# Kernel optimization log

Hardware: AMD Instinct MI355X
Metric: run time of the kernel (lower is better)

Reference implementation:

```python
import jax, jax.numpy as jnp
import numpy as np
import math

B, S, D, H = 16, 256, 1024, 16
DK = D // H
MAXLEN = 512


def _sinusoid_table(maxlen, dim):
    # rows for positions -maxlen .. maxlen-1  (2*maxlen rows)
    pos = jnp.arange(-maxlen, maxlen, dtype=jnp.float32)[:, None]
    i = jnp.arange(dim)
    angle = pos / jnp.power(10000.0, (2 * (i // 2)) / dim).astype(jnp.float32)
    return jnp.where(i % 2 == 0, jnp.sin(angle), jnp.cos(angle))


def setup_inputs() -> dict:
    key = jax.random.key(0)
    ks = jax.random.split(key, 13)
    std_qk = math.sqrt(2.0 / (D + DK))
    inp = {
        "x": jax.random.normal(ks[0], (B, S, D), jnp.float32),
        "Wq": jax.random.normal(ks[1], (D, D), jnp.float32) * std_qk,
        "bq": jnp.zeros((D,), jnp.float32),
        "Wk": jax.random.normal(ks[2], (D, D), jnp.float32) * std_qk,
        "bk": jnp.zeros((D,), jnp.float32),
        "Wv": jax.random.normal(ks[3], (D, D), jnp.float32) * std_qk,
        "bv": jnp.zeros((D,), jnp.float32),
        "Wr": jax.random.normal(ks[4], (D, D), jnp.float32) * std_qk,
        "br": jnp.zeros((D,), jnp.float32),
        "u_bias": jax.random.normal(ks[5], (H, DK), jnp.float32) * math.sqrt(2.0 / (H + DK)),
        "v_bias": jax.random.normal(ks[6], (H, DK), jnp.float32) * math.sqrt(2.0 / (H + DK)),
        "Wo": jax.random.normal(ks[7], (D, D), jnp.float32) * math.sqrt(2.0 / (D + D)),
        "bo": jnp.zeros((D,), jnp.float32),
    }
    return inp


def reference(x, Wq, bq, Wk, bk, Wv, bv, Wr, br, u_bias, v_bias, Wo, bo):
    table = _sinusoid_table(MAXLEN, D)  # (2*MAXLEN, D)
    # relative position indices: idx[s, z] = z - s, shifted by +MAXLEN
    relpos_idx = (jnp.arange(2 * S)[None, :] - jnp.arange(S)[:, None])[:, :S] + MAXLEN
    relpos_vec = table[relpos_idx]  # (S, S, D)

    q = (x @ Wq.T + bq).reshape(B, S, H, DK)
    k = (x @ Wk.T + bk).reshape(B, S, H, DK)
    v = (x @ Wv.T + bv).reshape(B, S, H, DK)

    rp_k = (relpos_vec @ Wk.T + bk).reshape(S, S, H, DK)       # shared k_proj
    kR = (x @ Wr.T + br).reshape(B, S, H, DK)                  # relpos_k_proj(keys)
    rp_R = (relpos_vec @ Wr.T + br).reshape(S, S, H, DK)       # relpos_k_proj(relpos)

    w = jnp.einsum('bshd,bzhd->bhsz', q, k)
    w = w + jnp.einsum('bshd,szhd->bhsz', q, rp_k)
    w = w + jnp.einsum('hd,bzhd->bhz', u_bias, kR)[:, :, None, :]
    w = w + jnp.einsum('hd,szhd->hsz', v_bias, rp_R)[None, :, :, :]
    w = w / math.sqrt(DK)

    causal = jnp.tril(jnp.ones((S, S), jnp.float32))[None, None, :, :]
    w = w + jnp.log(causal)  # -inf above diagonal

    attn = jax.nn.softmax(w, axis=-1)                          # (B,H,S,S)
    vw = jnp.einsum('bhsz,bzhd->bshd', attn, v).reshape(B, S, D)
    return vw @ Wo.T + bo
```

## Files before the change

kernel.cpp:

```cpp
#include <hip/hip_runtime.h>
#include <math.h>

constexpr int kB  = 16;
constexpr int kS  = 256;
constexpr int kD  = 1024;
constexpr int kH  = 16;
constexpr float kScale = 0.125f;

using bf16x8  = __attribute__((ext_vector_type(8))) short;
using floatx4 = __attribute__((ext_vector_type(4))) float;
typedef unsigned short u16;

__device__ __forceinline__ u16 f2bf(float x) {
  union { float f; unsigned u; } v; v.f = x;
  unsigned r = v.u + 0x7fffu + ((v.u >> 16) & 1u);
  return (u16)(r >> 16);
}
__device__ __forceinline__ float bf2f(u16 h) {
  union { unsigned u; float f; } v; v.u = ((unsigned)h) << 16;
  return v.f;
}

#define MFMA16(a, b, c) __builtin_amdgcn_mfma_f32_16x16x32_bf16((a), (b), (c), 0, 0, 0)
#define GLL16(gp, lp)                                                        \
  __builtin_amdgcn_global_load_lds(                                          \
      (const __attribute__((address_space(1))) unsigned int*)(gp),           \
      (__attribute__((address_space(3))) unsigned int*)(lp), 16, 0, 0)

__global__ __launch_bounds__(256) void pack_k(
    const float* __restrict__ x, const float* __restrict__ Wq,
    const float* __restrict__ Wk, const float* __restrict__ Wv,
    const float* __restrict__ Wo,
    const float* __restrict__ bq, const float* __restrict__ bk,
    const float* __restrict__ bv,
    const float* __restrict__ Wr, const float* __restrict__ br,
    const float* __restrict__ ub, const float* __restrict__ vb,
    u16* __restrict__ xA, u16* __restrict__ W3b, u16* __restrict__ Wob,
    float* __restrict__ b3) {
  if (blockIdx.x >= 8451) {
    int gid = (blockIdx.x - 8451) * 256 + threadIdx.x;
    int j = gid >> 10, c = gid & 1023;
    int h = j & 15;
    const float* bvec = (j < 16 ? ub : vb) + h * 64;
    const float* wcol = Wr + (size_t)(h * 64) * 1024 + c;
    float a = 0.f;
#pragma unroll
    for (int d = 0; d < 64; ++d) a += bvec[d] * wcol[(size_t)d * 1024];
    W3b[(size_t)(3072 + j) * 1024 + c] = f2bf(a);
    if (gid < 128) {
      float s = 0.f;
      if (gid < 32) {
        const float* bv2 = (gid < 16 ? ub : vb) + (gid & 15) * 64;
        const float* brp = br + (gid & 15) * 64;
        for (int d = 0; d < 64; ++d) s += bv2[d] * brp[d];
      }
      b3[3072 + gid] = s;
    }
    return;
  }
  size_t i = ((size_t)blockIdx.x * 256 + threadIdx.x) * 4;
  const size_t NX = (size_t)4194304, NW = (size_t)1048576;
  const size_t BEND = NX + 4 * NW + 3072;
  const float* src;
  u16* dst;
  size_t o;
  if (i < NX) {
    src = x; dst = xA; o = i;
  } else if (i < NX + 3 * NW) {
    size_t j = i - NX;
    int sel = (int)(j >> 20);
    o = j & (NW - 1);
    src = sel == 0 ? Wq : sel == 1 ? Wv : Wk;
    dst = W3b + (size_t)sel * NW;
  } else if (i < NX + 4 * NW) {
    o = i - NX - 3 * NW;
    src = Wo; dst = Wob;
  } else if (i < BEND) {
    size_t j = i - NX - 4 * NW;
    int sel = (int)(j >> 10);
    o = j & 1023;
    src = sel == 0 ? bq : sel == 1 ? bv : bk;
    *reinterpret_cast<float4*>(b3 + j) = *reinterpret_cast<const float4*>(src + o);
    return;
  } else if (i < BEND + 262144) {
    size_t j = i - BEND;
    int p = (int)(j >> 10);
    int ibase = (int)(j & 1023);
    ushort4 r;
    u16* rr = (u16*)&r;
#pragma unroll
    for (int c = 0; c < 4; ++c) {
      int idx = ibase + c;
      float ex = (float)(2 * (idx / 2)) * (1.0f / 1024.0f);
      float scale = exp2f(ex * -13.287712379549449f);
      float angle = (float)(p - 255) * scale;
      rr[c] = f2bf((idx & 1) ? cosf(angle) : sinf(angle));
    }
    *reinterpret_cast<ushort4*>(xA + NX + j) = r;
    return;
  } else {
    return;
  }
  float4 v = *reinterpret_cast<const float4*>(src + o);
  ushort4 r;
  r.x = f2bf(v.x); r.y = f2bf(v.y); r.z = f2bf(v.z); r.w = f2bf(v.w);
  *reinterpret_cast<ushort4*>(dst + o) = r;
}

__global__ __launch_bounds__(256) void gemm_k(
    const u16* __restrict__ A, const u16* __restrict__ W,
    const float* __restrict__ bias, float* __restrict__ Cv,
    int M, int N, int K, int mTiles, int nTiles) {
  const int xcd = blockIdx.x & 7;
  const int li  = blockIdx.x >> 3;
  const int r0   = (xcd * mTiles) >> 3;
  const int rcnt = (((xcd + 1) * mTiles) >> 3) - r0;
  if (li >= rcnt * nTiles) return;
  const int bm = (r0 + li % rcnt) * 128;
  const int bn = (li / rcnt) * 128;

  __shared__ u16 Alds[2][128 * 64];
  __shared__ u16 Blds[2][128 * 64];
  const int t = threadIdx.x, w = t >> 6, l = t & 63;
  const int l15 = l & 15, quad = l >> 4;
  const int wm = w >> 1, wn = w & 1;
  const int lrow8 = l >> 3;
  const int kslot = l & 7;
  const int NT = K >> 6;

  floatx4 acc[4][4] = {};

  auto stage = [&](int kt) {
    const int buf = kt & 1, k0 = kt << 6;
#pragma unroll
    for (int sg = 0; sg < 4; ++sg) {
      int mrow = sg * 32 + w * 8 + lrow8;
      int gk = (kslot ^ (mrow & 7)) << 3;
      GLL16(A + (size_t)(bm + mrow) * K + k0 + gk, Alds[buf] + (sg * 32 + w * 8) * 64);
      GLL16(W + (size_t)(bn + mrow) * K + k0 + gk, Blds[buf] + (sg * 32 + w * 8) * 64);
    }
  };

  stage(0);
  asm volatile("s_waitcnt vmcnt(0)" ::: "memory");
  __syncthreads();

  for (int kt = 0; kt < NT; ++kt) {
    if (kt + 1 < NT) stage(kt + 1);
    const u16* AL = Alds[kt & 1];
    const u16* BL = Blds[kt & 1];
#pragma unroll
    for (int c = 0; c < 2; ++c) {
      bf16x8 af[4], bf[4];
#pragma unroll
      for (int mi = 0; mi < 4; ++mi) {
        int am = wm * 64 + mi * 16 + l15;
        af[mi] = *(const bf16x8*)(AL + am * 64 + (((c * 4 + quad) ^ (am & 7)) << 3));
      }
#pragma unroll
      for (int ni = 0; ni < 4; ++ni) {
        int an = wn * 64 + ni * 16 + l15;
        bf[ni] = *(const bf16x8*)(BL + an * 64 + (((c * 4 + quad) ^ (an & 7)) << 3));
      }
#pragma unroll
      for (int mi = 0; mi < 4; ++mi)
#pragma unroll
        for (int ni = 0; ni < 4; ++ni)
          acc[mi][ni] = MFMA16(af[mi], bf[ni], acc[mi][ni]);
    }
    asm volatile("s_waitcnt vmcnt(0)" ::: "memory");
    __syncthreads();
  }

#pragma unroll
  for (int ni = 0; ni < 4; ++ni) {
    int col = bn + wn * 64 + ni * 16 + l15;
    float bv = bias[col];
#pragma unroll
    for (int mi = 0; mi < 4; ++mi) {
      int mrow = bm + wm * 64 + mi * 16 + quad * 4;
#pragma unroll
      for (int r = 0; r < 4; ++r) {
        Cv[(size_t)(mrow + r) * N + col] = acc[mi][ni][r] + bv;
      }
    }
  }
}

#define PHASE_MFMA(aa, bb, mh, nh, LG)                                         \
  do {                                                                         \
    __builtin_amdgcn_s_barrier();                                              \
    asm volatile("s_waitcnt lgkmcnt(" #LG ")" ::: "memory");                   \
    __builtin_amdgcn_sched_barrier(0);                                         \
    __builtin_amdgcn_s_setprio(1);                                             \
    _Pragma("unroll") for (int kc = 0; kc < 2; ++kc)                           \
        _Pragma("unroll") for (int i = 0; i < 4; ++i)                          \
            _Pragma("unroll") for (int j = 0; j < 2; ++j)                      \
                acc[(mh) * 4 + i][(nh) * 2 + j] = MFMA16(                      \
                    aa[kc][i], bb[kc][j], acc[(mh) * 4 + i][(nh) * 2 + j]);    \
    __builtin_amdgcn_s_setprio(0);                                             \
  } while (0)

__global__ __launch_bounds__(512, 2) void gemm256_k(
    const u16* __restrict__ A, const u16* __restrict__ W,
    const float* __restrict__ bias, u16* __restrict__ Cv,
    int K, float* __restrict__ utb, float* __restrict__ dtb,
    int mTiles, int nTiles) {
  const int nwg = mTiles * nTiles;
  const int qq = nwg >> 3, rr8 = nwg & 7;
  const int xcd = blockIdx.x & 7;
  const int wgid = (xcd < rr8 ? xcd * (qq + 1) : rr8 * (qq + 1) + (xcd - rr8) * qq)
                   + (blockIdx.x >> 3);
  const int bm = (wgid / nTiles) * 256;
  const int bn = (wgid % nTiles) * 256;

  __shared__ u16 lds[2 * 32768];

  const int t = threadIdx.x, w = t >> 6, l = t & 63;
  const int l15 = l & 15, quad = l >> 4;
  const int wm = w >> 2, wn = w & 3;

  const int NT = K >> 6;
  floatx4 acc[8][4] = {};

  auto stage = [&](int kt, int h) {
    const u16* srcm = (h < 2) ? A : W;
    const int baser = ((h < 2) ? bm : bn) + (h & 1) * 128;
    u16* dst = lds + (kt & 1) * 32768 + h * 8192 + w * 512;
    const int k0 = kt << 6;
#pragma unroll
    for (int j = 0; j < 2; ++j) {
      int sub = w * 8 + (l >> 3) + j * 64;
      int gk = ((l & 7) ^ (sub & 7)) << 3;
      GLL16(srcm + (size_t)(baser + sub) * K + k0 + gk, dst + j * 4096);
    }
  };

  bf16x8 a0[2][4], a1[2][4], b0[2][2], b1[2][2];

  auto readA = [&](bf16x8 (&aa)[2][4], const u16* LA, int hh) {
#pragma unroll
    for (int i = 0; i < 4; ++i) {
      int am = wm * 128 + hh * 64 + i * 16 + l15;
      const u16* p = LA + am * 64;
      aa[0][i] = *(const bf16x8*)(p + ((quad ^ (am & 7)) << 3));
      aa[1][i] = *(const bf16x8*)(p + (((4 + quad) ^ (am & 7)) << 3));
    }
  };
  auto readB = [&](bf16x8 (&bb)[2][2], const u16* LB, int hh) {
#pragma unroll
    for (int j = 0; j < 2; ++j) {
      int an = wn * 64 + hh * 32 + j * 16 + l15;
      const u16* p = LB + an * 64;
      bb[0][j] = *(const bf16x8*)(p + ((quad ^ (an & 7)) << 3));
      bb[1][j] = *(const bf16x8*)(p + (((4 + quad) ^ (an & 7)) << 3));
    }
  };

  stage(0, 2); stage(0, 3); stage(0, 0); stage(0, 1);
  stage(1, 2); stage(1, 3); stage(1, 0);
  asm volatile("s_waitcnt vmcnt(6)" ::: "memory");
  __builtin_amdgcn_s_barrier();
  readA(a0, lds, 0);
  readB(b0, lds + 16384, 0);

  for (int kt = 0; kt < NT; ++kt) {
    const u16* LA = lds + (kt & 1) * 32768;
    const u16* LB = LA + 16384;

    readB(b1, LB, 1);
    if (kt + 1 < NT) stage(kt + 1, 1);
    PHASE_MFMA(a0, b0, 0, 0, 4);
    __builtin_amdgcn_s_barrier();

    readA(a1, LA, 1);
    PHASE_MFMA(a0, b1, 0, 1, 8);
    __builtin_amdgcn_s_barrier();

    if (kt + 2 < NT) stage(kt + 2, 2);
    PHASE_MFMA(a1, b0, 1, 0, 0);
    __builtin_amdgcn_s_barrier();

    if (kt + 2 < NT) {
      stage(kt + 2, 3); stage(kt + 2, 0);
      asm volatile("s_waitcnt vmcnt(6)" ::: "memory");
    } else {
      asm volatile("s_waitcnt vmcnt(0)" ::: "memory");
    }
    __builtin_amdgcn_s_barrier();
    asm volatile("s_waitcnt lgkmcnt(0)" ::: "memory");
    __builtin_amdgcn_sched_barrier(0);
    if (kt + 1 < NT) {
      const u16* LAn = lds + ((kt + 1) & 1) * 32768;
      readA(a0, LAn, 0);
      readB(b0, LAn + 16384, 0);
    }
    __builtin_amdgcn_s_setprio(1);
#pragma unroll
    for (int kc = 0; kc < 2; ++kc)
#pragma unroll
      for (int i = 0; i < 4; ++i)
#pragma unroll
        for (int j = 0; j < 2; ++j)
          acc[4 + i][2 + j] = MFMA16(a1[kc][i], b1[kc][j], acc[4 + i][2 + j]);
    __builtin_amdgcn_s_setprio(0);
    __builtin_amdgcn_s_barrier();
  }

  float* fl = (float*)lds;
  u16* VTp = Cv + (size_t)4194304;
#pragma unroll 1
  for (int half = 0; half < 2; ++half) {
    __syncthreads();
    if (wm == half) {
#pragma unroll
      for (int ni = 0; ni < 4; ++ni) {
        float bv = bias[bn + wn * 64 + ni * 16 + l15];
#pragma unroll
        for (int mi = 0; mi < 8; ++mi) {
#pragma unroll
          for (int r = 0; r < 4; ++r) {
            int lr = mi * 16 + quad * 4 + r;
            int c  = wn * 64 + ni * 16 + l15;
            int key = ((r ^ quad) & 3) << 4;
            fl[lr * 256 + (c ^ key)] = acc[mi][ni][r] + bv;
          }
        }
      }
    }
    __syncthreads();
    if (bn >= 1024 && bn < 2048) {
      if (bm < 4096) {
        int bb = bm >> 8;
        int c = (w & 3) * 64 + l;
        int rbase = (w >> 2) * 64;
        int col = bn + c;
        int hh2 = (col >> 6) & 15;
        u16* vpb = VTp + ((size_t)((bb << 4) + hh2) * 64 + (col & 63)) * 256 +
                   half * 128 + rbase;
#pragma unroll 1
        for (int pp = 0; pp < 8; ++pp) {
          int rb = rbase + pp * 8;
          u16 hv[8];
#pragma unroll
          for (int e = 0; e < 8; ++e) {
            int lr = rb + e;
            int key = ((lr & 3) ^ ((lr >> 2) & 3)) << 4;
            hv[e] = f2bf(fl[lr * 256 + (c ^ key)]);
          }
          *(ushort4*)(vpb + pp * 8) = *(ushort4*)&hv[0];
          *(ushort4*)(vpb + pp * 8 + 4) = *(ushort4*)&hv[4];
        }
      }
    } else {
#pragma unroll 1
      for (int cc = 0; cc < 4; ++cc) {
        int col0 = bn + cc * 64;
#pragma unroll
        for (int rr = 0; rr < 4; ++rr) {
          int lr = w * 16 + rr * 4 + quad;
          int key = ((rr ^ quad) & 3) << 4;
          float4 v = *(const float4*)&fl[lr * 256 + ((cc * 64 + (l15 << 2)) ^ key)];
          int grow = bm + half * 128 + lr;
          if (col0 < 3072) {
            ushort4 hvv;
            hvv.x = f2bf(v.x); hvv.y = f2bf(v.y); hvv.z = f2bf(v.z); hvv.w = f2bf(v.w);
            int matsel = col0 >> 10;
            int hh2 = (col0 >> 6) & 15;
            if (grow < 4096) {
              int bb = grow >> 8, ss = grow & 255;
              *(ushort4*)(Cv + (size_t)matsel * 4194304 +
                          ((size_t)(((bb << 4) + hh2) << 8) + ss) * 64 + (l15 << 2)) = hvv;
            } else if (matsel == 2) {
              int pp = grow - 4096;
              *(ushort4*)(Cv + (size_t)3 * 4194304 +
                          ((size_t)((hh2 << 8) + pp)) * 64 + (l15 << 2)) = hvv;
            }
          } else if (col0 < 3104) {
#pragma unroll
            for (int e = 0; e < 4; ++e) {
              int col = col0 + (l15 << 2) + e;
              float vv = e == 0 ? v.x : e == 1 ? v.y : e == 2 ? v.z : v.w;
              if (col < 3088) {
                if (grow < 4096)
                  utb[((grow >> 8) * 16 + (col - 3072)) * 256 + (grow & 255)] = vv;
              } else if (col < 3104) {
                if (grow >= 4096)
                  dtb[(col - 3088) * 256 + (grow - 4096)] = vv;
              }
            }
          }
        }
      }
    }
  }
}

__global__ __launch_bounds__(512, 2) void attn_k(
    const u16* __restrict__ Qh, const u16* __restrict__ Kh,
    const u16* __restrict__ VT, const u16* __restrict__ RPKh,
    const float* __restrict__ ut, const float* __restrict__ dt,
    u16* __restrict__ vw) {
  __shared__ float ScW[8][16 * 260];
  __shared__ float Ut[256], Dt[256];

  const int bh = blockIdx.x;
  const int h = bh & 15;
  const int b = bh >> 4;
  const size_t bh256 = (size_t)bh << 8;

  const int t = threadIdx.x, w = t >> 6, l = t & 63;
  const int l15 = l & 15, quad = l >> 4;

  if (t < 256) Ut[t] = ut[bh256 + t];
  else         Dt[t - 256] = dt[((size_t)h << 8) + (t - 256)];
  __syncthreads();

  float* scw = &ScW[w][0];

#pragma unroll 1
  for (int sidx = 0; sidx < 2; ++sidx) {
    const int s = sidx ? (15 - w) : w;
    const int rB = s << 4;

    bf16x8 qa0, qa1;
    {
      const u16* qp = Qh + (bh256 + rB + l15) * 64 + quad * 8;
      qa0 = *(const bf16x8*)qp;
      qa1 = *(const bf16x8*)(qp + 32);
    }
    bf16x8 kA0, kA1, kB0, kB1, rA0, rA1, rB0, rB1;
    {
      const u16* kp = Kh + (bh256 + l15) * 64 + quad * 8;
      kA0 = *(const bf16x8*)kp;
      kA1 = *(const bf16x8*)(kp + 32);
      const u16* rp = RPKh + (((size_t)h << 8) + 240 - rB + l15) * 64 + quad * 8;
      rA0 = *(const bf16x8*)rp;
      rA1 = *(const bf16x8*)(rp + 32);
    }

#pragma unroll
    for (int j = 0; j < 16; ++j) {
      if (j > s) break;
      if (j + 1 <= s) {
        const u16* kp = Kh + (bh256 + ((j + 1) << 4) + l15) * 64 + quad * 8;
        const u16* rp = RPKh + (((size_t)h << 8) + 240 - rB + ((j + 1) << 4) + l15) * 64 + quad * 8;
        if ((j + 1) & 1) {
          kB0 = *(const bf16x8*)kp; kB1 = *(const bf16x8*)(kp + 32);
          rB0 = *(const bf16x8*)rp; rB1 = *(const bf16x8*)(rp + 32);
        } else {
          kA0 = *(const bf16x8*)kp; kA1 = *(const bf16x8*)(kp + 32);
          rA0 = *(const bf16x8*)rp; rA1 = *(const bf16x8*)(rp + 32);
        }
      }
      bf16x8 k0 = (j & 1) ? kB0 : kA0;
      bf16x8 k1 = (j & 1) ? kB1 : kA1;
      bf16x8 r0 = (j & 1) ? rB0 : rA0;
      bf16x8 r1 = (j & 1) ? rB1 : rA1;
      {
        floatx4 acc = {};
        acc = MFMA16(qa0, k0, acc);
        acc = MFMA16(qa1, k1, acc);
        float u = Ut[(j << 4) + l15];
#pragma unroll
        for (int r = 0; r < 4; ++r)
          scw[(4 * quad + r) * 260 + (j << 4) + l15] = acc[r] + u;
      }
      {
        floatx4 acc = {};
        acc = MFMA16(qa0, r0, acc);
        acc = MFMA16(qa1, r1, acc);
        float dv = Dt[240 - rB + (j << 4) + l15];
#pragma unroll
        for (int r = 0; r < 4; ++r) {
          int z = (j << 4) + l15 + 4 * quad + r - 15;
          if (z >= 0)
            scw[(4 * quad + r) * 260 + z] += acc[r] + dv;
        }
      }
    }

    const int kcmax = s >> 1;
    const int Rabs = rB + l15;
    float m = -1e30f;
#pragma unroll
    for (int kc = 0; kc < 8; ++kc) {
      if (kc > kcmax) break;
      const float* sp = scw + l15 * 260 + kc * 32 + quad * 8;
      floatx4 v0 = *(const floatx4*)sp;
      floatx4 v1 = *(const floatx4*)(sp + 4);
#pragma unroll
      for (int e = 0; e < 4; ++e) {
        int z = kc * 32 + quad * 8 + e;
        if (z <= Rabs) m = fmaxf(m, v0[e]);
        if (z + 4 <= Rabs) m = fmaxf(m, v1[e]);
      }
    }
    m = fmaxf(m, __shfl_xor(m, 16));
    m = fmaxf(m, __shfl_xor(m, 32));
    m *= kScale;

    floatx4 oacc[4] = {};
    float sum = 0.f;
    bf16x8 vA[4], vB[4];
    {
      const u16* vp = VT + ((size_t)bh * 64 + l15) * 256 + quad * 8;
#pragma unroll
      for (int nt = 0; nt < 4; ++nt)
        vA[nt] = *(const bf16x8*)(vp + (size_t)nt * 16 * 256);
    }
#pragma unroll
    for (int kc = 0; kc < 8; ++kc) {
      if (kc > kcmax) break;
      if (kc + 1 <= kcmax) {
        const u16* vp = VT + ((size_t)bh * 64 + l15) * 256 + (kc + 1) * 32 + quad * 8;
        if ((kc + 1) & 1) {
#pragma unroll
          for (int nt = 0; nt < 4; ++nt)
            vB[nt] = *(const bf16x8*)(vp + (size_t)nt * 16 * 256);
        } else {
#pragma unroll
          for (int nt = 0; nt < 4; ++nt)
            vA[nt] = *(const bf16x8*)(vp + (size_t)nt * 16 * 256);
        }
      }
      const float* sp = scw + l15 * 260 + kc * 32 + quad * 8;
      floatx4 v0 = *(const floatx4*)sp;
      floatx4 v1 = *(const floatx4*)(sp + 4);
      bf16x8 pa;
#pragma unroll
      for (int e = 0; e < 4; ++e) {
        int z = kc * 32 + quad * 8 + e;
        float p0 = (z <= Rabs) ? __expf(v0[e] * kScale - m) : 0.f;
        float p1 = (z + 4 <= Rabs) ? __expf(v1[e] * kScale - m) : 0.f;
        sum += p0 + p1;
        pa[e] = (short)f2bf(p0);
        pa[e + 4] = (short)f2bf(p1);
      }
#pragma unroll
      for (int nt = 0; nt < 4; ++nt)
        oacc[nt] = MFMA16(pa, (kc & 1) ? vB[nt] : vA[nt], oacc[nt]);
    }
    sum += __shfl_xor(sum, 16);
    sum += __shfl_xor(sum, 32);
    float rinv = 1.f / sum;

#pragma unroll
    for (int r = 0; r < 4; ++r) {
      float rs = __shfl(rinv, 4 * quad + r);
      int row = rB + 4 * quad + r;
#pragma unroll
      for (int nt = 0; nt < 4; ++nt)
        vw[(size_t)(b * 256 + row) * 1024 + h * 64 + nt * 16 + l15] =
            f2bf(oacc[nt][r] * rs);
    }
  }
}

extern "C" void kernel_launch(void* const* d_in, const int* in_sizes, int n_in,
                              void* d_out, int out_size, void* d_ws, size_t ws_size,
                              hipStream_t stream) {
  const float* x  = (const float*)d_in[0];
  const float* Wq = (const float*)d_in[1];
  const float* bq = (const float*)d_in[2];
  const float* Wk = (const float*)d_in[3];
  const float* bk = (const float*)d_in[4];
  const float* Wv = (const float*)d_in[5];
  const float* bv = (const float*)d_in[6];
  const float* Wr = (const float*)d_in[7];
  const float* br = (const float*)d_in[8];
  const float* ub = (const float*)d_in[9];
  const float* vb = (const float*)d_in[10];
  const float* Wo = (const float*)d_in[11];
  const float* bo = (const float*)d_in[12];
  float* out = (float*)d_out;

  char* base = (char*)d_ws;
  size_t off = 0;
  auto alloc = [&](size_t bytes) {
    void* p = base + off;
    off += (bytes + 255) & ~(size_t)255;
    return p;
  };

  const size_t MAT = (size_t)4194304;
  u16*   xA    = (u16*)alloc((size_t)4352 * 1024 * 2);
  u16*   W3b   = (u16*)alloc((size_t)3328 * 1024 * 2);
  u16*   Wob   = (u16*)alloc((size_t)1024 * 1024 * 2);
  float* b3    = (float*)alloc((size_t)3328 * 4);
  u16*   Ph    = (u16*)alloc((3 * MAT + 262144) * 2);
  float* utb   = (float*)alloc((size_t)65536 * 4);
  float* dtb   = (float*)alloc((size_t)4096 * 4);
  u16*   vwb   = (u16*)alloc((size_t)4096 * 1024 * 2);

  u16* Qh   = Ph;
  u16* VTb  = Ph + MAT;
  u16* Kh   = Ph + 2 * MAT;
  u16* RPKh = Ph + 3 * MAT;

  pack_k<<<dim3(8579), dim3(256), 0, stream>>>(x, Wq, Wk, Wv, Wo, bq, bk, bv,
                                               Wr, br, ub, vb,
                                               xA, W3b, Wob, b3);

  gemm256_k<<<dim3(221), dim3(512), 0, stream>>>(xA, W3b, b3, Ph,
                                                 1024, utb, dtb, 17, 13);

  attn_k<<<dim3(256), dim3(512), 0, stream>>>(Qh, Kh, VTb, RPKh, utb, dtb, vwb);

  gemm_k<<<dim3(256), dim3(256), 0, stream>>>(vwb, Wob, bo, out,
                                              4096, 1024, 1024, 32, 8);
}
```

Baseline: 195.9 us.

## Replace 256x256 pipelined projection GEMM with simpler 128x128 double-buffered kernel

Swaps the fused QKV/relpos projection GEMM from 256x256 tiles with 8 waves and a hand-scheduled four-phase MFMA pipeline to 128x128 tiles with 4 waves and a plain double-buffered loop. The launch grows from 221 to 884 workgroups, so all CUs get work and the last wave is less uneven. The cost is lower operand reuse per tile and a full vmcnt(0) wait plus barrier each K step, which gives up the finer load/compute overlap. The epilogue is rewritten for the smaller tile.

```diff
diff --git a/kernel.cpp b/kernel.cpp
--- a/kernel.cpp
+++ b/kernel.cpp
@@ -187,21 +187,7 @@
   }
 }
 
-#define PHASE_MFMA(aa, bb, mh, nh, LG)                                         \
-  do {                                                                         \
-    __builtin_amdgcn_s_barrier();                                              \
-    asm volatile("s_waitcnt lgkmcnt(" #LG ")" ::: "memory");                   \
-    __builtin_amdgcn_sched_barrier(0);                                         \
-    __builtin_amdgcn_s_setprio(1);                                             \
-    _Pragma("unroll") for (int kc = 0; kc < 2; ++kc)                           \
-        _Pragma("unroll") for (int i = 0; i < 4; ++i)                          \
-            _Pragma("unroll") for (int j = 0; j < 2; ++j)                      \
-                acc[(mh) * 4 + i][(nh) * 2 + j] = MFMA16(                      \
-                    aa[kc][i], bb[kc][j], acc[(mh) * 4 + i][(nh) * 2 + j]);    \
-    __builtin_amdgcn_s_setprio(0);                                             \
-  } while (0)
-
-__global__ __launch_bounds__(512, 2) void gemm256_k(
+__global__ __launch_bounds__(256) void gemmqvk_k(
     const u16* __restrict__ A, const u16* __restrict__ W,
     const float* __restrict__ bias, u16* __restrict__ Cv,
     int K, float* __restrict__ utb, float* __restrict__ dtb,
@@ -211,183 +197,140 @@
   const int xcd = blockIdx.x & 7;
   const int wgid = (xcd < rr8 ? xcd * (qq + 1) : rr8 * (qq + 1) + (xcd - rr8) * qq)
                    + (blockIdx.x >> 3);
-  const int bm = (wgid / nTiles) * 256;
-  const int bn = (wgid % nTiles) * 256;
-
-  __shared__ u16 lds[2 * 32768];
+  const int bm = (wgid / nTiles) * 128;
+  const int bn = (wgid % nTiles) * 128;
+
+  __shared__ u16 lds[32768];
 
   const int t = threadIdx.x, w = t >> 6, l = t & 63;
   const int l15 = l & 15, quad = l >> 4;
-  const int wm = w >> 2, wn = w & 3;
-
+  const int wm = w >> 1, wn = w & 1;
+  const int lrow8 = l >> 3;
+  const int kslot = l & 7;
   const int NT = K >> 6;
-  floatx4 acc[8][4] = {};
-
-  auto stage = [&](int kt, int h) {
-    const u16* srcm = (h < 2) ? A : W;
-    const int baser = ((h < 2) ? bm : bn) + (h & 1) * 128;
-    u16* dst = lds + (kt & 1) * 32768 + h * 8192 + w * 512;
+
+  floatx4 acc[4][4] = {};
+
+  auto stage = [&](int kt) {
     const int k0 = kt << 6;
-#pragma unroll
-    for (int j = 0; j < 2; ++j) {
-      int sub = w * 8 + (l >> 3) + j * 64;
-      int gk = ((l & 7) ^ (sub & 7)) << 3;
-      GLL16(srcm + (size_t)(baser + sub) * K + k0 + gk, dst + j * 4096);
+    u16* base = lds + (kt & 1) * 16384;
+#pragma unroll
+    for (int sg = 0; sg < 4; ++sg) {
+      int mrow = sg * 32 + w * 8 + lrow8;
+      int gk = (kslot ^ (mrow & 7)) << 3;
+      GLL16(A + (size_t)(bm + mrow) * K + k0 + gk, base + (sg * 32 + w * 8) * 64);
+      GLL16(W + (size_t)(bn + mrow) * K + k0 + gk, base + 8192 + (sg * 32 + w * 8) * 64);
     }
   };
 
-  bf16x8 a0[2][4], a1[2][4], b0[2][2], b1[2][2];
-
-  auto readA = [&](bf16x8 (&aa)[2][4], const u16* LA, int hh) {
-#pragma unroll
-    for (int i = 0; i < 4; ++i) {
-      int am = wm * 128 + hh * 64 + i * 16 + l15;
-      const u16* p = LA + am * 64;
-      aa[0][i] = *(const bf16x8*)(p + ((quad ^ (am & 7)) << 3));
-      aa[1][i] = *(const bf16x8*)(p + (((4 + quad) ^ (am & 7)) << 3));
-    }
-  };
-  auto readB = [&](bf16x8 (&bb)[2][2], const u16* LB, int hh) {
-#pragma unroll
-    for (int j = 0; j < 2; ++j) {
-      int an = wn * 64 + hh * 32 + j * 16 + l15;
-      const u16* p = LB + an * 64;
-      bb[0][j] = *(const bf16x8*)(p + ((quad ^ (an & 7)) << 3));
-      bb[1][j] = *(const bf16x8*)(p + (((4 + quad) ^ (an & 7)) << 3));
-    }
-  };
-
-  stage(0, 2); stage(0, 3); stage(0, 0); stage(0, 1);
-  stage(1, 2); stage(1, 3); stage(1, 0);
-  asm volatile("s_waitcnt vmcnt(6)" ::: "memory");
-  __builtin_amdgcn_s_barrier();
-  readA(a0, lds, 0);
-  readB(b0, lds + 16384, 0);
+  stage(0);
+  asm volatile("s_waitcnt vmcnt(0)" ::: "memory");
+  __syncthreads();
 
   for (int kt = 0; kt < NT; ++kt) {
-    const u16* LA = lds + (kt & 1) * 32768;
-    const u16* LB = LA + 16384;
-
-    readB(b1, LB, 1);
-    if (kt + 1 < NT) stage(kt + 1, 1);
-    PHASE_MFMA(a0, b0, 0, 0, 4);
-    __builtin_amdgcn_s_barrier();
-
-    readA(a1, LA, 1);
-    PHASE_MFMA(a0, b1, 0, 1, 8);
-    __builtin_amdgcn_s_barrier();
-
-    if (kt + 2 < NT) stage(kt + 2, 2);
-    PHASE_MFMA(a1, b0, 1, 0, 0);
-    __builtin_amdgcn_s_barrier();
-
-    if (kt + 2 < NT) {
-      stage(kt + 2, 3); stage(kt + 2, 0);
-      asm volatile("s_waitcnt vmcnt(6)" ::: "memory");
-    } else {
-      asm volatile("s_waitcnt vmcnt(0)" ::: "memory");
-    }
-    __builtin_amdgcn_s_barrier();
-    asm volatile("s_waitcnt lgkmcnt(0)" ::: "memory");
-    __builtin_amdgcn_sched_barrier(0);
-    if (kt + 1 < NT) {
-      const u16* LAn = lds + ((kt + 1) & 1) * 32768;
-      readA(a0, LAn, 0);
-      readB(b0, LAn + 16384, 0);
-    }
-    __builtin_amdgcn_s_setprio(1);
-#pragma unroll
-    for (int kc = 0; kc < 2; ++kc)
-#pragma unroll
-      for (int i = 0; i < 4; ++i)
-#pragma unroll
-        for (int j = 0; j < 2; ++j)
-          acc[4 + i][2 + j] = MFMA16(a1[kc][i], b1[kc][j], acc[4 + i][2 + j]);
-    __builtin_amdgcn_s_setprio(0);
-    __builtin_amdgcn_s_barrier();
+    if (kt + 1 < NT) stage(kt + 1);
+    const u16* AL = lds + (kt & 1) * 16384;
+    const u16* BL = AL + 8192;
+#pragma unroll
+    for (int c = 0; c < 2; ++c) {
+      bf16x8 af[4], bf[4];
+#pragma unroll
+      for (int mi = 0; mi < 4; ++mi) {
+        int am = wm * 64 + mi * 16 + l15;
+        af[mi] = *(const bf16x8*)(AL + am * 64 + (((c * 4 + quad) ^ (am & 7)) << 3));
+      }
+#pragma unroll
+      for (int ni = 0; ni < 4; ++ni) {
+        int an = wn * 64 + ni * 16 + l15;
+        bf[ni] = *(const bf16x8*)(BL + an * 64 + (((c * 4 + quad) ^ (an & 7)) << 3));
+      }
+#pragma unroll
+      for (int mi = 0; mi < 4; ++mi)
+#pragma unroll
+        for (int ni = 0; ni < 4; ++ni)
+          acc[mi][ni] = MFMA16(af[mi], bf[ni], acc[mi][ni]);
+    }
+    asm volatile("s_waitcnt vmcnt(0)" ::: "memory");
+    __syncthreads();
   }
 
   float* fl = (float*)lds;
+#pragma unroll
+  for (int ni = 0; ni < 4; ++ni) {
+    float bv = bias[bn + wn * 64 + ni * 16 + l15];
+#pragma unroll
+    for (int mi = 0; mi < 4; ++mi) {
+#pragma unroll
+      for (int r = 0; r < 4; ++r) {
+        int lr = wm * 64 + mi * 16 + quad * 4 + r;
+        int c  = wn * 64 + ni * 16 + l15;
+        int key = ((r ^ quad) & 3) << 4;
+        fl[lr * 128 + (c ^ key)] = acc[mi][ni][r] + bv;
+      }
+    }
+  }
+  __syncthreads();
+
   u16* VTp = Cv + (size_t)4194304;
+  if (bn >= 1024 && bn < 2048) {
+    if (bm < 4096) {
+      int bb = bm >> 8;
+      int zb = bm & 128;
+      int c = (w & 1) * 64 + l;
+      int rbase = (w >> 1) * 64;
+      int col = bn + c;
+      int hh2 = (col >> 6) & 15;
+      u16* vpb = VTp + ((size_t)((bb << 4) + hh2) * 64 + (col & 63)) * 256 +
+                 zb + rbase;
 #pragma unroll 1
-  for (int half = 0; half < 2; ++half) {
-    __syncthreads();
-    if (wm == half) {
-#pragma unroll
-      for (int ni = 0; ni < 4; ++ni) {
-        float bv = bias[bn + wn * 64 + ni * 16 + l15];
-#pragma unroll
-        for (int mi = 0; mi < 8; ++mi) {
-#pragma unroll
-          for (int r = 0; r < 4; ++r) {
-            int lr = mi * 16 + quad * 4 + r;
-            int c  = wn * 64 + ni * 16 + l15;
-            int key = ((r ^ quad) & 3) << 4;
-            fl[lr * 256 + (c ^ key)] = acc[mi][ni][r] + bv;
+      for (int pp = 0; pp < 8; ++pp) {
+        int rb = rbase + pp * 8;
+        u16 hv[8];
+#pragma unroll
+        for (int e = 0; e < 8; ++e) {
+          int lr = rb + e;
+          int key = ((lr & 3) ^ ((lr >> 2) & 3)) << 4;
+          hv[e] = f2bf(fl[lr * 128 + (c ^ key)]);
+        }
+        *(ushort4*)(vpb + pp * 8) = *(ushort4*)&hv[0];
+        *(ushort4*)(vpb + pp * 8 + 4) = *(ushort4*)&hv[4];
+      }
+    }
+  } else {
+#pragma unroll 1
+    for (int cc = 0; cc < 2; ++cc) {
+      int col0 = bn + cc * 64;
+#pragma unroll
+      for (int rr = 0; rr < 8; ++rr) {
+        int lr = w * 32 + rr * 4 + quad;
+        int key = ((rr ^ quad) & 3) << 4;
+        float4 v = *(const float4*)&fl[lr * 128 + ((cc * 64 + (l15 << 2)) ^ key)];
+        int grow = bm + lr;
+        if (col0 < 3072) {
+          ushort4 hvv;
+          hvv.x = f2bf(v.x); hvv.y = f2bf(v.y); hvv.z = f2bf(v.z); hvv.w = f2bf(v.w);
+          int matsel = col0 >> 10;
+          int hh2 = (col0 >> 6) & 15;
+          if (grow < 4096) {
+            int bb = grow >> 8, ss = grow & 255;
+            *(ushort4*)(Cv + (size_t)matsel * 4194304 +
+                        ((size_t)(((bb << 4) + hh2) << 8) + ss) * 64 + (l15 << 2)) = hvv;
+          } else if (matsel == 2) {
+            int pp = grow - 4096;
+            *(ushort4*)(Cv + (size_t)3 * 4194304 +
+                        ((size_t)((hh2 << 8) + pp)) * 64 + (l15 << 2)) = hvv;
           }
-        }
-      }
-    }
-    __syncthreads();
-    if (bn >= 1024 && bn < 2048) {
-      if (bm < 4096) {
-        int bb = bm >> 8;
-        int c = (w & 3) * 64 + l;
-        int rbase = (w >> 2) * 64;
-        int col = bn + c;
-        int hh2 = (col >> 6) & 15;
-        u16* vpb = VTp + ((size_t)((bb << 4) + hh2) * 64 + (col & 63)) * 256 +
-                   half * 128 + rbase;
-#pragma unroll 1
-        for (int pp = 0; pp < 8; ++pp) {
-          int rb = rbase + pp * 8;
-          u16 hv[8];
-#pragma unroll
-          for (int e = 0; e < 8; ++e) {
-            int lr = rb + e;
-            int key = ((lr & 3) ^ ((lr >> 2) & 3)) << 4;
-            hv[e] = f2bf(fl[lr * 256 + (c ^ key)]);
-          }
-          *(ushort4*)(vpb + pp * 8) = *(ushort4*)&hv[0];
-          *(ushort4*)(vpb + pp * 8 + 4) = *(ushort4*)&hv[4];
-        }
-      }
-    } else {
-#pragma unroll 1
-      for (int cc = 0; cc < 4; ++cc) {
-        int col0 = bn + cc * 64;
-#pragma unroll
-        for (int rr = 0; rr < 4; ++rr) {
-          int lr = w * 16 + rr * 4 + quad;
-          int key = ((rr ^ quad) & 3) << 4;
-          float4 v = *(const float4*)&fl[lr * 256 + ((cc * 64 + (l15 << 2)) ^ key)];
-          int grow = bm + half * 128 + lr;
-          if (col0 < 3072) {
-            ushort4 hvv;
-            hvv.x = f2bf(v.x); hvv.y = f2bf(v.y); hvv.z = f2bf(v.z); hvv.w = f2bf(v.w);
-            int matsel = col0 >> 10;
-            int hh2 = (col0 >> 6) & 15;
-            if (grow < 4096) {
-              int bb = grow >> 8, ss = grow & 255;
-              *(ushort4*)(Cv + (size_t)matsel * 4194304 +
-                          ((size_t)(((bb << 4) + hh2) << 8) + ss) * 64 + (l15 << 2)) = hvv;
-            } else if (matsel == 2) {
-              int pp = grow - 4096;
-              *(ushort4*)(Cv + (size_t)3 * 4194304 +
-                          ((size_t)((hh2 << 8) + pp)) * 64 + (l15 << 2)) = hvv;
-            }
-          } else if (col0 < 3104) {
-#pragma unroll
-            for (int e = 0; e < 4; ++e) {
-              int col = col0 + (l15 << 2) + e;
-              float vv = e == 0 ? v.x : e == 1 ? v.y : e == 2 ? v.z : v.w;
-              if (col < 3088) {
-                if (grow < 4096)
-                  utb[((grow >> 8) * 16 + (col - 3072)) * 256 + (grow & 255)] = vv;
-              } else if (col < 3104) {
-                if (grow >= 4096)
-                  dtb[(col - 3088) * 256 + (grow - 4096)] = vv;
-              }
+        } else if (col0 < 3104) {
+#pragma unroll
+          for (int e = 0; e < 4; ++e) {
+            int col = col0 + (l15 << 2) + e;
+            float vv = e == 0 ? v.x : e == 1 ? v.y : e == 2 ? v.z : v.w;
+            if (col < 3088) {
+              if (grow < 4096)
+                utb[((grow >> 8) * 16 + (col - 3072)) * 256 + (grow & 255)] = vv;
+            } else if (col < 3104) {
+              if (grow >= 4096)
+                dtb[(col - 3088) * 256 + (grow - 4096)] = vv;
             }
           }
         }
@@ -602,8 +545,8 @@
                                                Wr, br, ub, vb,
                                                xA, W3b, Wob, b3);
 
-  gemm256_k<<<dim3(221), dim3(512), 0, stream>>>(xA, W3b, b3, Ph,
-                                                 1024, utb, dtb, 17, 13);
+  gemmqvk_k<<<dim3(884), dim3(256), 0, stream>>>(xA, W3b, b3, Ph,
+                                                 1024, utb, dtb, 34, 26);
 
   attn_k<<<dim3(256), dim3(512), 0, stream>>>(Qh, Kh, VTb, RPKh, utb, dtb, vwb);
 
```

Result: faster. 189.1 us (-3.5%).
